# Kernel optimization log

Hardware: AMD Instinct MI355X
Metric: run time of the kernel (lower is better)

The kernel has to match this reference:

```python
import jax, jax.numpy as jnp
import numpy as np

IMAGE_SIZE = 512
STRIDES = (8, 16, 32)
W_SEG, W_DET, W_CLS = 1.0, 1.0, 0.5


def _bce_logits(x, y):
    # numerically stable binary cross entropy with logits (broadcasts y)
    return jnp.maximum(x, 0.0) - x * y + jnp.log1p(jnp.exp(-jnp.abs(x)))


def _focal_loss_mean(logits, targets, num_classes, alpha=0.25, gamma=2.0):
    # sigmoid focal loss; targets are class indices, -1 (or any negative) => all-background row
    t = jax.nn.one_hot(targets, num_classes, dtype=logits.dtype)
    p = jax.nn.sigmoid(logits)
    ce = _bce_logits(logits, t)
    p_t = p * t + (1.0 - p) * (1.0 - t)
    a_t = alpha * t + (1.0 - alpha) * (1.0 - t)
    return jnp.mean(a_t * (1.0 - p_t) ** gamma * ce)


def _det_scale_loss(cls_logits, reg_preds, cent_preds, boxes, labels, stride):
    B, Cp1, H, W = cls_logits.shape
    C = Cp1 - 1
    L = H * W
    cls = jnp.transpose(cls_logits, (0, 2, 3, 1))[..., 1:].reshape(B, L, C)
    reg = jnp.transpose(reg_preds, (0, 2, 3, 1)).reshape(B, L, 4)
    cent = cent_preds.reshape(B, L)
    xs = (jnp.arange(W, dtype=jnp.float32) + 0.5) * stride
    ys = (jnp.arange(H, dtype=jnp.float32) + 0.5) * stride
    gy, gx = jnp.meshgrid(ys, xs, indexing='ij')
    loc_x = gx.reshape(-1)
    loc_y = gy.reshape(-1)

    def per_image(cls_i, reg_i, cent_i, gb, gl):
        b = gb * IMAGE_SIZE  # [cx,cy,w,h] in pixels
        x0 = b[:, 0] - b[:, 2] * 0.5
        y0 = b[:, 1] - b[:, 3] * 0.5
        x1 = b[:, 0] + b[:, 2] * 0.5
        y1 = b[:, 1] + b[:, 3] * 0.5
        l = loc_x[:, None] - x0[None, :]
        t = loc_y[:, None] - y0[None, :]
        r = x1[None, :] - loc_x[:, None]
        btm = y1[None, :] - loc_y[:, None]
        ltrb = jnp.stack([l, t, r, btm], axis=-1)  # (L, N, 4)
        inside = jnp.min(ltrb, axis=-1) > 0
        area = (x1 - x0) * (y1 - y0)
        masked_area = jnp.where(inside, area[None, :], jnp.inf)
        idx = jnp.argmin(masked_area, axis=-1)  # min-area matched box per location
        pos = jnp.any(inside, axis=-1)
        cls_t = jnp.where(pos, gl[idx], -1)
        reg_t = jnp.take_along_axis(ltrb, idx[:, None, None], axis=1)[:, 0, :] / stride
        lr = reg_t[:, jnp.array([0, 2])]
        tb = reg_t[:, jnp.array([1, 3])]
        eps = 1e-6
        cen_t = jnp.sqrt(jnp.clip((jnp.min(lr, -1) / (jnp.max(lr, -1) + eps)) * (jnp.min(tb, -1) / (jnp.max(tb, -1) + eps)), 0.0, 1.0))
        cls_l = _focal_loss_mean(cls_i, cls_t, C)
        npos = jnp.sum(pos)
        d = reg_i - reg_t
        sl1 = jnp.mean(jnp.where(jnp.abs(d) < 1.0, 0.5 * d * d, jnp.abs(d) - 0.5), axis=-1)
        posf = pos.astype(jnp.float32)
        denom = jnp.maximum(npos, 1).astype(jnp.float32)
        reg_l = jnp.where(npos > 0, jnp.sum(sl1 * posf) / denom, 0.0)
        bce = _bce_logits(cent_i, cen_t)
        cen_l = jnp.where(npos > 0, jnp.sum(bce * posf) / denom, 0.0)
        return cls_l, reg_l, cen_l

    cl, rl, cel = jax.vmap(per_image)(cls, reg, cent, boxes, labels)
    return jnp.mean(cl), jnp.mean(rl), jnp.mean(cel)


def _total_loss(seg_logits, seg_mask, cls_list, reg_list, cen_list, boxes, labels, cls_pred, cls_target):
    # segmentation: BCE-with-logits, integer mask broadcast as float target over channels
    seg_t = seg_mask.astype(jnp.float32)[:, None, :, :]  # (B,1,H,W) broadcasts vs (B,C,H,W)
    seg_loss = jnp.mean(_bce_logits(seg_logits, seg_t))
    tot_cls = 0.0
    tot_reg = 0.0
    tot_cen = 0.0
    for s in range(3):
        cl, rl, cel = _det_scale_loss(cls_list[s], reg_list[s], cen_list[s], boxes, labels, STRIDES[s])
        tot_cls = tot_cls + cl
        tot_reg = tot_reg + rl
        tot_cen = tot_cen + cel
    n = 3.0
    det_loss = tot_cls / n + tot_reg / n + tot_cen / n
    cls_loss = _focal_loss_mean(cls_pred, cls_target, cls_pred.shape[-1])
    return W_SEG * seg_loss + W_DET * det_loss + W_CLS * cls_loss


def setup_inputs() -> dict:
    key = jax.random.key(0)
    ks = jax.random.split(key, 16)
    B = 32
    inp = {
        'seg_logits': jax.random.normal(ks[0], (B, 4, 512, 512), jnp.float32),
        'seg_mask': jax.random.randint(ks[1], (B, 512, 512), 0, 4, jnp.int32),
        'cls_logits_s0': jax.random.normal(ks[2], (B, 5, 64, 64), jnp.float32),
        'cls_logits_s1': jax.random.normal(ks[3], (B, 5, 32, 32), jnp.float32),
        'cls_logits_s2': jax.random.normal(ks[4], (B, 5, 16, 16), jnp.float32),
        'reg_preds_s0': jax.random.normal(ks[5], (B, 4, 64, 64), jnp.float32),
        'reg_preds_s1': jax.random.normal(ks[6], (B, 4, 32, 32), jnp.float32),
        'reg_preds_s2': jax.random.normal(ks[7], (B, 4, 16, 16), jnp.float32),
        'centerness_s0': jax.random.normal(ks[8], (B, 1, 64, 64), jnp.float32),
        'centerness_s1': jax.random.normal(ks[9], (B, 1, 32, 32), jnp.float32),
        'centerness_s2': jax.random.normal(ks[10], (B, 1, 16, 16), jnp.float32),
        'boxes': jax.random.uniform(ks[11], (B, 20, 4), jnp.float32),
        'labels': jax.random.randint(ks[12], (B, 20), 0, 4, jnp.int32),
        'cls_pred': jax.random.normal(ks[13], (B, 10), jnp.float32),
        'cls_target': jax.random.randint(ks[14], (B,), 0, 10, jnp.int32),
    }
    return inp


def reference(seg_logits, seg_mask, cls_logits_s0, cls_logits_s1, cls_logits_s2, reg_preds_s0, reg_preds_s1, reg_preds_s2, centerness_s0, centerness_s1, centerness_s2, boxes, labels, cls_pred, cls_target):
    return _total_loss(seg_logits, seg_mask,
                       (cls_logits_s0, cls_logits_s1, cls_logits_s2),
                       (reg_preds_s0, reg_preds_s1, reg_preds_s2),
                       (centerness_s0, centerness_s1, centerness_s2),
                       boxes, labels, cls_pred, cls_target)
```

## Files before the change

### kernel.cpp

```cpp
#include <hip/hip_runtime.h>
#include <math.h>

#define NB 32
#define SEG_BLOCKS 2048
#define DET_BLOCKS 96


__device__ __forceinline__ float bce_logits(float x, float y) {
    float a = fabsf(x);
    return fmaxf(x, 0.f) - x * y + __logf(1.f + __expf(-a));
}

__device__ __forceinline__ float focal_elt(float x, float t) {
    float p = 1.f / (1.f + __expf(-x));
    float ce = bce_logits(x, t);
    float p_t = (t > 0.5f) ? p : (1.f - p);
    float a_t = (t > 0.5f) ? 0.25f : 0.75f;
    float om = 1.f - p_t;
    return a_t * om * om * ce;
}

template <int N>
__device__ void blk_reduce_arr(float* v) {
    __shared__ float sm[N][4];
    int lane = threadIdx.x & 63;
    int wid  = threadIdx.x >> 6;
#pragma unroll
    for (int j = 0; j < N; j++) {
        float x = v[j];
#pragma unroll
        for (int off = 32; off > 0; off >>= 1) x += __shfl_down(x, off, 64);
        if (lane == 0) sm[j][wid] = x;
    }
    __syncthreads();
    if (threadIdx.x == 0) {
#pragma unroll
        for (int j = 0; j < N; j++) {
            float s = 0.f;
#pragma unroll
            for (int w = 0; w < 4; w++) s += sm[j][w];
            v[j] = s;
        }
    }
}


__global__ __launch_bounds__(256) void fused_kernel(
        const float* __restrict__ seg_logits, const int* __restrict__ mask,
        const float* __restrict__ cls0, const float* __restrict__ cls1, const float* __restrict__ cls2,
        const float* __restrict__ reg0, const float* __restrict__ reg1, const float* __restrict__ reg2,
        const float* __restrict__ cen0, const float* __restrict__ cen1, const float* __restrict__ cen2,
        const float* __restrict__ boxes, const int* __restrict__ labels,
        float* __restrict__ segpart, float* __restrict__ detc) {

    if (blockIdx.x < DET_BLOCKS) {
        const int s = blockIdx.x >> 5;
        const int b = blockIdx.x & 31;
        int Wd, shift, L; float stride;
        const float *cls, *reg, *cen;
        if (s == 0)      { Wd = 64; shift = 6; L = 4096; stride = 8.f;  cls = cls0; reg = reg0; cen = cen0; }
        else if (s == 1) { Wd = 32; shift = 5; L = 1024; stride = 16.f; cls = cls1; reg = reg1; cen = cen1; }
        else             { Wd = 16; shift = 4; L = 256;  stride = 32.f; cls = cls2; reg = reg2; cen = cen2; }

        __shared__ float sx0[20], sy0[20], sx1[20], sy1[20], sar[20];
        __shared__ int   slb[20];
        if (threadIdx.x < 20) {
            int k = threadIdx.x;
            const float* bb = boxes + (b * 20 + k) * 4;
            float cx = bb[0] * 512.f, cy = bb[1] * 512.f;
            float w  = bb[2] * 512.f, h  = bb[3] * 512.f;
            float x0 = cx - 0.5f * w, y0 = cy - 0.5f * h;
            float x1 = cx + 0.5f * w, y1 = cy + 0.5f * h;
            sx0[k] = x0; sy0[k] = y0; sx1[k] = x1; sy1[k] = y1;
            sar[k] = (x1 - x0) * (y1 - y0);
            slb[k] = labels[b * 20 + k];
        }
        __syncthreads();

        const float* clsb = cls + (size_t)b * 5 * L;
        const float* regb = reg + (size_t)b * 4 * L;
        const float* cenb = cen + (size_t)b * L;
        const float inv = 1.f / stride;

        float cls_s = 0.f, reg_s = 0.f, cen_s = 0.f, np = 0.f;
        for (int l = threadIdx.x; l < L; l += 256) {
            float lx = ((l & (Wd - 1)) + 0.5f) * stride;
            float ly = ((l >> shift)   + 0.5f) * stride;
            int bk = -1; float ba = INFINITY;
            float bl = 0.f, btp = 0.f, brr = 0.f, bbt = 0.f;
#pragma unroll
            for (int k = 0; k < 20; k++) {
                float li = lx - sx0[k], ti = ly - sy0[k];
                float ri = sx1[k] - lx, bi = sy1[k] - ly;
                float mn = fminf(fminf(li, ti), fminf(ri, bi));
                if (mn > 0.f && sar[k] < ba) {
                    ba = sar[k]; bk = k;
                    bl = li; btp = ti; brr = ri; bbt = bi;
                }
            }
            int tl = (bk >= 0) ? slb[bk] : -1;
#pragma unroll
            for (int c = 0; c < 4; c++) {
                float x = clsb[(c + 1) * L + l];
                cls_s += focal_elt(x, (c == tl) ? 1.f : 0.f);
            }
            if (bk >= 0) {
                float r0 = bl * inv, r1 = btp * inv, r2 = brr * inv, r3 = bbt * inv;
                float d0 = regb[0 * L + l] - r0;
                float d1 = regb[1 * L + l] - r1;
                float d2 = regb[2 * L + l] - r2;
                float d3 = regb[3 * L + l] - r3;
                float a0 = fabsf(d0), a1 = fabsf(d1), a2 = fabsf(d2), a3 = fabsf(d3);
                float sl = (a0 < 1.f ? 0.5f * d0 * d0 : a0 - 0.5f)
                         + (a1 < 1.f ? 0.5f * d1 * d1 : a1 - 0.5f)
                         + (a2 < 1.f ? 0.5f * d2 * d2 : a2 - 0.5f)
                         + (a3 < 1.f ? 0.5f * d3 * d3 : a3 - 0.5f);
                reg_s += 0.25f * sl;
                float mnlr = fminf(r0, r2), mxlr = fmaxf(r0, r2);
                float mntb = fminf(r1, r3), mxtb = fmaxf(r1, r3);
                float v = (mnlr / (mxlr + 1e-6f)) * (mntb / (mxtb + 1e-6f));
                v = fminf(fmaxf(v, 0.f), 1.f);
                float ct = sqrtf(v);
                cen_s += bce_logits(cenb[l], ct);
                np += 1.f;
            }
        }

        float v4[4] = {cls_s, reg_s, cen_s, np};
        blk_reduce_arr<4>(v4);
        if (threadIdx.x == 0) {
            float cls_l = v4[0] / (L * 4.f);
            float npos  = v4[3];
            float denom = fmaxf(npos, 1.f);
            float reg_l = (npos > 0.f) ? v4[1] / denom : 0.f;
            float cen_l = (npos > 0.f) ? v4[2] / denom : 0.f;
            detc[blockIdx.x] = (cls_l + reg_l + cen_l) * (1.f / (float)DET_BLOCKS);
        }
        __syncthreads();
    }

    const int HW  = 512 * 512;
    const int QPI = HW / 4;
    const int TOTQ = NB * QPI;
    int tid = blockIdx.x * 256 + threadIdx.x;
    float acc = 0.f;
    for (int q = tid; q < TOTQ; q += SEG_BLOCKS * 256) {
        int b   = q >> 16;
        int hwq = q & 65535;
        const int4 m4 = ((const int4*)(mask + (size_t)b * HW))[hwq];
        float ty0 = (float)m4.x, ty1 = (float)m4.y, ty2 = (float)m4.z, ty3 = (float)m4.w;
        const float4* base = (const float4*)(seg_logits + (size_t)b * 4 * HW);
#pragma unroll
        for (int c = 0; c < 4; c++) {
            float4 x4 = base[c * QPI + hwq];
            acc += bce_logits(x4.x, ty0) + bce_logits(x4.y, ty1)
                 + bce_logits(x4.z, ty2) + bce_logits(x4.w, ty3);
        }
    }
    float v[1] = {acc};
    blk_reduce_arr<1>(v);
    if (threadIdx.x == 0) segpart[blockIdx.x] = v[0];
}


__global__ __launch_bounds__(256) void final_kernel(
        const float* __restrict__ segpart, const float* __restrict__ detc,
        const float* __restrict__ cls_pred, const int* __restrict__ cls_target,
        float* __restrict__ out) {
    const float seg_scale = 1.f / 33554432.f;
    const float cls_scale = 0.5f / 320.f;
    float acc = 0.f;
    for (int i = threadIdx.x; i < SEG_BLOCKS; i += 256) acc += segpart[i] * seg_scale;
    if (threadIdx.x < DET_BLOCKS) acc += detc[threadIdx.x];
    for (int e = threadIdx.x; e < NB * 10; e += 256) {
        int i = e / 10, c = e - i * 10;
        acc += cls_scale * focal_elt(cls_pred[e], (cls_target[i] == c) ? 1.f : 0.f);
    }
    float v[1] = {acc};
    blk_reduce_arr<1>(v);
    if (threadIdx.x == 0) out[0] = v[0];
}


extern "C" void kernel_launch(void* const* d_in, const int* in_sizes, int n_in,
                              void* d_out, int out_size, void* d_ws, size_t ws_size,
                              hipStream_t stream) {
    const float* seg_logits = (const float*)d_in[0];
    const int*   seg_mask   = (const int*)d_in[1];
    const float* cls0 = (const float*)d_in[2];
    const float* cls1 = (const float*)d_in[3];
    const float* cls2 = (const float*)d_in[4];
    const float* reg0 = (const float*)d_in[5];
    const float* reg1 = (const float*)d_in[6];
    const float* reg2 = (const float*)d_in[7];
    const float* cen0 = (const float*)d_in[8];
    const float* cen1 = (const float*)d_in[9];
    const float* cen2 = (const float*)d_in[10];
    const float* boxes  = (const float*)d_in[11];
    const int*   labels = (const int*)d_in[12];
    const float* cls_pred   = (const float*)d_in[13];
    const int*   cls_target = (const int*)d_in[14];

    float* ws      = (float*)d_ws;
    float* segpart = ws;
    float* detc    = ws + SEG_BLOCKS;

    fused_kernel<<<SEG_BLOCKS, 256, 0, stream>>>(seg_logits, seg_mask,
                                                 cls0, cls1, cls2,
                                                 reg0, reg1, reg2,
                                                 cen0, cen1, cen2,
                                                 boxes, labels, segpart, detc);
    final_kernel<<<1, 256, 0, stream>>>(segpart, detc, cls_pred, cls_target,
                                        (float*)d_out);
}
```

Before: 248.0 us.

## Split detection and segmentation into dedicated blocks and batch segmentation loads

Detection blocks now return after their reduction instead of also doing a share of the segmentation work. The grid grows by the detection block count, and each segmentation block handles one contiguous 1024-quad chunk. Each thread issues all 4 mask loads and 16 logit loads up front before computing, replacing a grid-stride loop, to raise memory-level parallelism. This uses more registers per thread and relies on the total quad count exactly equalling SEG_BLOCKS*1024.

After: 256.7 us. +3.5%, slower.

```diff
diff --git a/kernel.cpp b/kernel.cpp
--- a/kernel.cpp
+++ b/kernel.cpp
@@ -2,8 +2,9 @@
 #include <math.h>
 
 #define NB 32
+#define DET_BLOCKS 96
 #define SEG_BLOCKS 2048
-#define DET_BLOCKS 96
+#define TOTAL_BLOCKS (DET_BLOCKS + SEG_BLOCKS)
 
 
 __device__ __forceinline__ float bce_logits(float x, float y) {
@@ -136,30 +137,44 @@
             float cen_l = (npos > 0.f) ? v4[2] / denom : 0.f;
             detc[blockIdx.x] = (cls_l + reg_l + cen_l) * (1.f / (float)DET_BLOCKS);
         }
-        __syncthreads();
+        return;
     }
 
     const int HW  = 512 * 512;
     const int QPI = HW / 4;
-    const int TOTQ = NB * QPI;
-    int tid = blockIdx.x * 256 + threadIdx.x;
+    const int sblk = blockIdx.x - DET_BLOCKS;
+    const size_t qbase = (size_t)sblk * 1024;
+    const int b   = (int)(qbase >> 16);
+    const int hw0 = (int)(qbase & 65535) + threadIdx.x;
+
+    const int4*   mb = (const int4*)(mask + (size_t)b * HW) + hw0;
+    const float4* xb = (const float4*)(seg_logits + (size_t)b * 4 * HW) + hw0;
+
+    int4   m[4];
+    float4 x[16];
+#pragma unroll
+    for (int u = 0; u < 4; u++) m[u] = mb[u * 256];
+#pragma unroll
+    for (int u = 0; u < 4; u++)
+#pragma unroll
+        for (int c = 0; c < 4; c++) x[u * 4 + c] = xb[c * QPI + u * 256];
+
     float acc = 0.f;
-    for (int q = tid; q < TOTQ; q += SEG_BLOCKS * 256) {
-        int b   = q >> 16;
-        int hwq = q & 65535;
-        const int4 m4 = ((const int4*)(mask + (size_t)b * HW))[hwq];
-        float ty0 = (float)m4.x, ty1 = (float)m4.y, ty2 = (float)m4.z, ty3 = (float)m4.w;
-        const float4* base = (const float4*)(seg_logits + (size_t)b * 4 * HW);
+#pragma unroll
+    for (int u = 0; u < 4; u++) {
+        float ty0 = (float)m[u].x, ty1 = (float)m[u].y;
+        float ty2 = (float)m[u].z, ty3 = (float)m[u].w;
 #pragma unroll
         for (int c = 0; c < 4; c++) {
-            float4 x4 = base[c * QPI + hwq];
-            acc += bce_logits(x4.x, ty0) + bce_logits(x4.y, ty1)
-                 + bce_logits(x4.z, ty2) + bce_logits(x4.w, ty3);
-        }
-    }
+            float4 v = x[u * 4 + c];
+            acc += bce_logits(v.x, ty0) + bce_logits(v.y, ty1)
+                 + bce_logits(v.z, ty2) + bce_logits(v.w, ty3);
+        }
+    }
+
     float v[1] = {acc};
     blk_reduce_arr<1>(v);
-    if (threadIdx.x == 0) segpart[blockIdx.x] = v[0];
+    if (threadIdx.x == 0) segpart[sblk] = v[0];
 }
 
 
@@ -205,11 +220,11 @@
     float* segpart = ws;
     float* detc    = ws + SEG_BLOCKS;
 
-    fused_kernel<<<SEG_BLOCKS, 256, 0, stream>>>(seg_logits, seg_mask,
-                                                 cls0, cls1, cls2,
-                                                 reg0, reg1, reg2,
-                                                 cen0, cen1, cen2,
-                                                 boxes, labels, segpart, detc);
+    fused_kernel<<<TOTAL_BLOCKS, 256, 0, stream>>>(seg_logits, seg_mask,
+                                                   cls0, cls1, cls2,
+                                                   reg0, reg1, reg2,
+                                                   cen0, cen1, cen2,
+                                                   boxes, labels, segpart, detc);
     final_kernel<<<1, 256, 0, stream>>>(segpart, detc, cls_pred, cls_target,
                                         (float*)d_out);
 }
```

## Double-buffer segmentation loads through LDS with async global_load_lds

Applied to the files above, without the earlier changes.

Each segmentation block now owns a contiguous range of 2048 quads. It streams the mask and four logit channels into a double-buffered LDS tile using 16-byte global_load_lds, waiting with explicit vmcnt so the next chunk's loads overlap the current chunk's BCE math. Detection blocks become separate blocks that return early instead of also doing segmentation work, and the grid grows to cover both. The 40KB of shared memory per block limits occupancy, and the hand-written waitcnt and M0 offsets depend on how the compiler orders the loads.

Measured after the change: 247.4 us. No clear change (-0.2%).

```diff
diff --git a/kernel.cpp b/kernel.cpp
--- a/kernel.cpp
+++ b/kernel.cpp
@@ -2,8 +2,10 @@
 #include <math.h>
 
 #define NB 32
-#define SEG_BLOCKS 2048
 #define DET_BLOCKS 96
+#define SEG_BLOCKS 1024
+#define CHUNKS 8
+#define TOTAL_BLOCKS (DET_BLOCKS + SEG_BLOCKS)
 
 
 __device__ __forceinline__ float bce_logits(float x, float y) {
@@ -44,6 +46,11 @@
     }
 }
 
+__device__ __forceinline__ void stage16(const void* g, void* l) {
+    __builtin_amdgcn_global_load_lds((const unsigned int*)g, (unsigned int*)l,
+                                     16, 0, 0);
+}
+
 
 __global__ __launch_bounds__(256) void fused_kernel(
         const float* __restrict__ seg_logits, const int* __restrict__ mask,
@@ -52,6 +59,8 @@
         const float* __restrict__ cen0, const float* __restrict__ cen1, const float* __restrict__ cen2,
         const float* __restrict__ boxes, const int* __restrict__ labels,
         float* __restrict__ segpart, float* __restrict__ detc) {
+
+    __shared__ float4 sbuf[2][5 * 256];
 
     if (blockIdx.x < DET_BLOCKS) {
         const int s = blockIdx.x >> 5;
@@ -136,30 +145,66 @@
             float cen_l = (npos > 0.f) ? v4[2] / denom : 0.f;
             detc[blockIdx.x] = (cls_l + reg_l + cen_l) * (1.f / (float)DET_BLOCKS);
         }
-        __syncthreads();
+        return;
     }
 
     const int HW  = 512 * 512;
     const int QPI = HW / 4;
-    const int TOTQ = NB * QPI;
-    int tid = blockIdx.x * 256 + threadIdx.x;
+    const int sblk = blockIdx.x - DET_BLOCKS;
+    const size_t qbase = (size_t)sblk * 2048;
+    const int b  = (int)(qbase >> 16);
+    const int qs = (int)(qbase & 65535);
+    const int t  = threadIdx.x;
+
+    const int4*   mq = (const int4*)(mask + (size_t)b * HW) + qs;
+    const float4* xq = (const float4*)(seg_logits + (size_t)b * 4 * HW) + qs;
+
+    const int wbyte = __builtin_amdgcn_readfirstlane((t >> 6) << 10);
+
+    #define STAGE(p, j) do {                                                         \
+        char* base = (char*)&sbuf[p][0];                                             \
+        stage16(mq + (j) * 256 + t,           base + 0 * 4096 + wbyte);              \
+        stage16(xq + 0 * QPI + (j) * 256 + t, base + 1 * 4096 + wbyte);              \
+        stage16(xq + 1 * QPI + (j) * 256 + t, base + 2 * 4096 + wbyte);              \
+        stage16(xq + 2 * QPI + (j) * 256 + t, base + 3 * 4096 + wbyte);              \
+        stage16(xq + 3 * QPI + (j) * 256 + t, base + 4 * 4096 + wbyte);              \
+    } while (0)
+
+    STAGE(0, 0);
+
     float acc = 0.f;
-    for (int q = tid; q < TOTQ; q += SEG_BLOCKS * 256) {
-        int b   = q >> 16;
-        int hwq = q & 65535;
-        const int4 m4 = ((const int4*)(mask + (size_t)b * HW))[hwq];
-        float ty0 = (float)m4.x, ty1 = (float)m4.y, ty2 = (float)m4.z, ty3 = (float)m4.w;
-        const float4* base = (const float4*)(seg_logits + (size_t)b * 4 * HW);
-#pragma unroll
-        for (int c = 0; c < 4; c++) {
-            float4 x4 = base[c * QPI + hwq];
-            acc += bce_logits(x4.x, ty0) + bce_logits(x4.y, ty1)
-                 + bce_logits(x4.z, ty2) + bce_logits(x4.w, ty3);
-        }
-    }
+    for (int j = 0; j < CHUNKS; j++) {
+        const int p = j & 1;
+        if (j + 1 < CHUNKS) {
+            STAGE(p ^ 1, j + 1);
+            asm volatile("s_waitcnt vmcnt(5)" ::: "memory");
+        } else {
+            asm volatile("s_waitcnt vmcnt(0)" ::: "memory");
+        }
+        __syncthreads();
+
+        const int4   m  = ((const int4*)&sbuf[p][0])[t];
+        const float4 x0 = sbuf[p][1 * 256 + t];
+        const float4 x1 = sbuf[p][2 * 256 + t];
+        const float4 x2 = sbuf[p][3 * 256 + t];
+        const float4 x3 = sbuf[p][4 * 256 + t];
+        const float t0 = (float)m.x, t1 = (float)m.y, t2 = (float)m.z, t3 = (float)m.w;
+        acc += bce_logits(x0.x, t0) + bce_logits(x0.y, t1)
+             + bce_logits(x0.z, t2) + bce_logits(x0.w, t3);
+        acc += bce_logits(x1.x, t0) + bce_logits(x1.y, t1)
+             + bce_logits(x1.z, t2) + bce_logits(x1.w, t3);
+        acc += bce_logits(x2.x, t0) + bce_logits(x2.y, t1)
+             + bce_logits(x2.z, t2) + bce_logits(x2.w, t3);
+        acc += bce_logits(x3.x, t0) + bce_logits(x3.y, t1)
+             + bce_logits(x3.z, t2) + bce_logits(x3.w, t3);
+
+        __syncthreads();
+    }
+    #undef STAGE
+
     float v[1] = {acc};
     blk_reduce_arr<1>(v);
-    if (threadIdx.x == 0) segpart[blockIdx.x] = v[0];
+    if (threadIdx.x == 0) segpart[sblk] = v[0];
 }
 
 
@@ -205,11 +250,11 @@
     float* segpart = ws;
     float* detc    = ws + SEG_BLOCKS;
 
-    fused_kernel<<<SEG_BLOCKS, 256, 0, stream>>>(seg_logits, seg_mask,
-                                                 cls0, cls1, cls2,
-                                                 reg0, reg1, reg2,
-                                                 cen0, cen1, cen2,
-                                                 boxes, labels, segpart, detc);
+    fused_kernel<<<TOTAL_BLOCKS, 256, 0, stream>>>(seg_logits, seg_mask,
+                                                   cls0, cls1, cls2,
+                                                   reg0, reg1, reg2,
+                                                   cen0, cen1, cen2,
+                                                   boxes, labels, segpart, detc);
     final_kernel<<<1, 256, 0, stream>>>(segpart, detc, cls_pred, cls_target,
                                         (float*)d_out);
 }
```

## Split fused kernel into separate seg and det kernels with one-shot seg blocks

Applied to the files above, without the earlier changes.

The fused kernel, in which the first 96 blocks also handled detection, is split into a dedicated segmentation kernel and a detection kernel launched back-to-back. The segmentation kernel now uses 8192 blocks where each thread handles exactly one float4 group with no grid-stride loop, and it carries occupancy launch bounds. The goal is to stop detection blocks from delaying the segmentation stream and to expose more memory-level parallelism. In exchange there is an extra kernel launch, the detection work is serialized after the seg kernel instead of overlapping with it, and the final reduction has four times as many partial sums to add.

After: 271.3 us. +9.4%, slower.

```diff
diff --git a/kernel.cpp b/kernel.cpp
--- a/kernel.cpp
+++ b/kernel.cpp
@@ -2,8 +2,8 @@
 #include <math.h>
 
 #define NB 32
-#define SEG_BLOCKS 2048
 #define DET_BLOCKS 96
+#define SEG_BLOCKS 8192
 
 
 __device__ __forceinline__ float bce_logits(float x, float y) {
@@ -45,121 +45,127 @@
 }
 
 
-__global__ __launch_bounds__(256) void fused_kernel(
-        const float* __restrict__ seg_logits, const int* __restrict__ mask,
+__global__ __launch_bounds__(256, 8) void seg_kernel(
+        const float* __restrict__ logits, const int* __restrict__ mask,
+        float* __restrict__ partial) {
+    const int HW  = 512 * 512;
+    const int QPI = HW / 4;
+    const int b  = blockIdx.x >> 8;
+    const int hw = ((blockIdx.x & 255) << 8) + threadIdx.x;
+
+    const int4 m4 = ((const int4*)(mask + (size_t)b * HW))[hw];
+    const float4* xb = (const float4*)(logits + (size_t)b * 4 * HW) + hw;
+    const float4 x0 = xb[0];
+    const float4 x1 = xb[QPI];
+    const float4 x2 = xb[2 * QPI];
+    const float4 x3 = xb[3 * QPI];
+
+    const float t0 = (float)m4.x, t1 = (float)m4.y;
+    const float t2 = (float)m4.z, t3 = (float)m4.w;
+    float acc;
+    acc  = bce_logits(x0.x, t0) + bce_logits(x0.y, t1)
+         + bce_logits(x0.z, t2) + bce_logits(x0.w, t3);
+    acc += bce_logits(x1.x, t0) + bce_logits(x1.y, t1)
+         + bce_logits(x1.z, t2) + bce_logits(x1.w, t3);
+    acc += bce_logits(x2.x, t0) + bce_logits(x2.y, t1)
+         + bce_logits(x2.z, t2) + bce_logits(x2.w, t3);
+    acc += bce_logits(x3.x, t0) + bce_logits(x3.y, t1)
+         + bce_logits(x3.z, t2) + bce_logits(x3.w, t3);
+
+    float v[1] = {acc};
+    blk_reduce_arr<1>(v);
+    if (threadIdx.x == 0) partial[blockIdx.x] = v[0];
+}
+
+
+__global__ __launch_bounds__(256) void det_kernel(
         const float* __restrict__ cls0, const float* __restrict__ cls1, const float* __restrict__ cls2,
         const float* __restrict__ reg0, const float* __restrict__ reg1, const float* __restrict__ reg2,
         const float* __restrict__ cen0, const float* __restrict__ cen1, const float* __restrict__ cen2,
         const float* __restrict__ boxes, const int* __restrict__ labels,
-        float* __restrict__ segpart, float* __restrict__ detc) {
-
-    if (blockIdx.x < DET_BLOCKS) {
-        const int s = blockIdx.x >> 5;
-        const int b = blockIdx.x & 31;
-        int Wd, shift, L; float stride;
-        const float *cls, *reg, *cen;
-        if (s == 0)      { Wd = 64; shift = 6; L = 4096; stride = 8.f;  cls = cls0; reg = reg0; cen = cen0; }
-        else if (s == 1) { Wd = 32; shift = 5; L = 1024; stride = 16.f; cls = cls1; reg = reg1; cen = cen1; }
-        else             { Wd = 16; shift = 4; L = 256;  stride = 32.f; cls = cls2; reg = reg2; cen = cen2; }
-
-        __shared__ float sx0[20], sy0[20], sx1[20], sy1[20], sar[20];
-        __shared__ int   slb[20];
-        if (threadIdx.x < 20) {
-            int k = threadIdx.x;
-            const float* bb = boxes + (b * 20 + k) * 4;
-            float cx = bb[0] * 512.f, cy = bb[1] * 512.f;
-            float w  = bb[2] * 512.f, h  = bb[3] * 512.f;
-            float x0 = cx - 0.5f * w, y0 = cy - 0.5f * h;
-            float x1 = cx + 0.5f * w, y1 = cy + 0.5f * h;
-            sx0[k] = x0; sy0[k] = y0; sx1[k] = x1; sy1[k] = y1;
-            sar[k] = (x1 - x0) * (y1 - y0);
-            slb[k] = labels[b * 20 + k];
-        }
-        __syncthreads();
-
-        const float* clsb = cls + (size_t)b * 5 * L;
-        const float* regb = reg + (size_t)b * 4 * L;
-        const float* cenb = cen + (size_t)b * L;
-        const float inv = 1.f / stride;
-
-        float cls_s = 0.f, reg_s = 0.f, cen_s = 0.f, np = 0.f;
-        for (int l = threadIdx.x; l < L; l += 256) {
-            float lx = ((l & (Wd - 1)) + 0.5f) * stride;
-            float ly = ((l >> shift)   + 0.5f) * stride;
-            int bk = -1; float ba = INFINITY;
-            float bl = 0.f, btp = 0.f, brr = 0.f, bbt = 0.f;
-#pragma unroll
-            for (int k = 0; k < 20; k++) {
-                float li = lx - sx0[k], ti = ly - sy0[k];
-                float ri = sx1[k] - lx, bi = sy1[k] - ly;
-                float mn = fminf(fminf(li, ti), fminf(ri, bi));
-                if (mn > 0.f && sar[k] < ba) {
-                    ba = sar[k]; bk = k;
-                    bl = li; btp = ti; brr = ri; bbt = bi;
-                }
+        float* __restrict__ detc) {
+    const int s = blockIdx.x >> 5;
+    const int b = blockIdx.x & 31;
+    int Wd, shift, L; float stride;
+    const float *cls, *reg, *cen;
+    if (s == 0)      { Wd = 64; shift = 6; L = 4096; stride = 8.f;  cls = cls0; reg = reg0; cen = cen0; }
+    else if (s == 1) { Wd = 32; shift = 5; L = 1024; stride = 16.f; cls = cls1; reg = reg1; cen = cen1; }
+    else             { Wd = 16; shift = 4; L = 256;  stride = 32.f; cls = cls2; reg = reg2; cen = cen2; }
+
+    __shared__ float sx0[20], sy0[20], sx1[20], sy1[20], sar[20];
+    __shared__ int   slb[20];
+    if (threadIdx.x < 20) {
+        int k = threadIdx.x;
+        const float* bb = boxes + (b * 20 + k) * 4;
+        float cx = bb[0] * 512.f, cy = bb[1] * 512.f;
+        float w  = bb[2] * 512.f, h  = bb[3] * 512.f;
+        float x0 = cx - 0.5f * w, y0 = cy - 0.5f * h;
+        float x1 = cx + 0.5f * w, y1 = cy + 0.5f * h;
+        sx0[k] = x0; sy0[k] = y0; sx1[k] = x1; sy1[k] = y1;
+        sar[k] = (x1 - x0) * (y1 - y0);
+        slb[k] = labels[b * 20 + k];
+    }
+    __syncthreads();
+
+    const float* clsb = cls + (size_t)b * 5 * L;
+    const float* regb = reg + (size_t)b * 4 * L;
+    const float* cenb = cen + (size_t)b * L;
+    const float inv = 1.f / stride;
+
+    float cls_s = 0.f, reg_s = 0.f, cen_s = 0.f, np = 0.f;
+    for (int l = threadIdx.x; l < L; l += 256) {
+        float lx = ((l & (Wd - 1)) + 0.5f) * stride;
+        float ly = ((l >> shift)   + 0.5f) * stride;
+        int bk = -1; float ba = INFINITY;
+        float bl = 0.f, btp = 0.f, brr = 0.f, bbt = 0.f;
+#pragma unroll
+        for (int k = 0; k < 20; k++) {
+            float li = lx - sx0[k], ti = ly - sy0[k];
+            float ri = sx1[k] - lx, bi = sy1[k] - ly;
+            float mn = fminf(fminf(li, ti), fminf(ri, bi));
+            if (mn > 0.f && sar[k] < ba) {
+                ba = sar[k]; bk = k;
+                bl = li; btp = ti; brr = ri; bbt = bi;
             }
-            int tl = (bk >= 0) ? slb[bk] : -1;
-#pragma unroll
-            for (int c = 0; c < 4; c++) {
-                float x = clsb[(c + 1) * L + l];
-                cls_s += focal_elt(x, (c == tl) ? 1.f : 0.f);
-            }
-            if (bk >= 0) {
-                float r0 = bl * inv, r1 = btp * inv, r2 = brr * inv, r3 = bbt * inv;
-                float d0 = regb[0 * L + l] - r0;
-                float d1 = regb[1 * L + l] - r1;
-                float d2 = regb[2 * L + l] - r2;
-                float d3 = regb[3 * L + l] - r3;
-                float a0 = fabsf(d0), a1 = fabsf(d1), a2 = fabsf(d2), a3 = fabsf(d3);
-                float sl = (a0 < 1.f ? 0.5f * d0 * d0 : a0 - 0.5f)
-                         + (a1 < 1.f ? 0.5f * d1 * d1 : a1 - 0.5f)
-                         + (a2 < 1.f ? 0.5f * d2 * d2 : a2 - 0.5f)
-                         + (a3 < 1.f ? 0.5f * d3 * d3 : a3 - 0.5f);
-                reg_s += 0.25f * sl;
-                float mnlr = fminf(r0, r2), mxlr = fmaxf(r0, r2);
-                float mntb = fminf(r1, r3), mxtb = fmaxf(r1, r3);
-                float v = (mnlr / (mxlr + 1e-6f)) * (mntb / (mxtb + 1e-6f));
-                v = fminf(fmaxf(v, 0.f), 1.f);
-                float ct = sqrtf(v);
-                cen_s += bce_logits(cenb[l], ct);
-                np += 1.f;
-            }
-        }
-
-        float v4[4] = {cls_s, reg_s, cen_s, np};
-        blk_reduce_arr<4>(v4);
-        if (threadIdx.x == 0) {
-            float cls_l = v4[0] / (L * 4.f);
-            float npos  = v4[3];
-            float denom = fmaxf(npos, 1.f);
-            float reg_l = (npos > 0.f) ? v4[1] / denom : 0.f;
-            float cen_l = (npos > 0.f) ? v4[2] / denom : 0.f;
-            detc[blockIdx.x] = (cls_l + reg_l + cen_l) * (1.f / (float)DET_BLOCKS);
-        }
-        __syncthreads();
-    }
-
-    const int HW  = 512 * 512;
-    const int QPI = HW / 4;
-    const int TOTQ = NB * QPI;
-    int tid = blockIdx.x * 256 + threadIdx.x;
-    float acc = 0.f;
-    for (int q = tid; q < TOTQ; q += SEG_BLOCKS * 256) {
-        int b   = q >> 16;
-        int hwq = q & 65535;
-        const int4 m4 = ((const int4*)(mask + (size_t)b * HW))[hwq];
-        float ty0 = (float)m4.x, ty1 = (float)m4.y, ty2 = (float)m4.z, ty3 = (float)m4.w;
-        const float4* base = (const float4*)(seg_logits + (size_t)b * 4 * HW);
+        }
+        int tl = (bk >= 0) ? slb[bk] : -1;
 #pragma unroll
         for (int c = 0; c < 4; c++) {
-            float4 x4 = base[c * QPI + hwq];
-            acc += bce_logits(x4.x, ty0) + bce_logits(x4.y, ty1)
-                 + bce_logits(x4.z, ty2) + bce_logits(x4.w, ty3);
-        }
-    }
-    float v[1] = {acc};
-    blk_reduce_arr<1>(v);
-    if (threadIdx.x == 0) segpart[blockIdx.x] = v[0];
+            float x = clsb[(c + 1) * L + l];
+            cls_s += focal_elt(x, (c == tl) ? 1.f : 0.f);
+        }
+        if (bk >= 0) {
+            float r0 = bl * inv, r1 = btp * inv, r2 = brr * inv, r3 = bbt * inv;
+            float d0 = regb[0 * L + l] - r0;
+            float d1 = regb[1 * L + l] - r1;
+            float d2 = regb[2 * L + l] - r2;
+            float d3 = regb[3 * L + l] - r3;
+            float a0 = fabsf(d0), a1 = fabsf(d1), a2 = fabsf(d2), a3 = fabsf(d3);
+            float sl = (a0 < 1.f ? 0.5f * d0 * d0 : a0 - 0.5f)
+                     + (a1 < 1.f ? 0.5f * d1 * d1 : a1 - 0.5f)
+                     + (a2 < 1.f ? 0.5f * d2 * d2 : a2 - 0.5f)
+                     + (a3 < 1.f ? 0.5f * d3 * d3 : a3 - 0.5f);
+            reg_s += 0.25f * sl;
+            float mnlr = fminf(r0, r2), mxlr = fmaxf(r0, r2);
+            float mntb = fminf(r1, r3), mxtb = fmaxf(r1, r3);
+            float v = (mnlr / (mxlr + 1e-6f)) * (mntb / (mxtb + 1e-6f));
+            v = fminf(fmaxf(v, 0.f), 1.f);
+            float ct = sqrtf(v);
+            cen_s += bce_logits(cenb[l], ct);
+            np += 1.f;
+        }
+    }
+
+    float v4[4] = {cls_s, reg_s, cen_s, np};
+    blk_reduce_arr<4>(v4);
+    if (threadIdx.x == 0) {
+        float cls_l = v4[0] / (L * 4.f);
+        float npos  = v4[3];
+        float denom = fmaxf(npos, 1.f);
+        float reg_l = (npos > 0.f) ? v4[1] / denom : 0.f;
+        float cen_l = (npos > 0.f) ? v4[2] / denom : 0.f;
+        detc[blockIdx.x] = (cls_l + reg_l + cen_l) * (1.f / (float)DET_BLOCKS);
+    }
 }
 
 
@@ -205,11 +211,11 @@
     float* segpart = ws;
     float* detc    = ws + SEG_BLOCKS;
 
-    fused_kernel<<<SEG_BLOCKS, 256, 0, stream>>>(seg_logits, seg_mask,
-                                                 cls0, cls1, cls2,
-                                                 reg0, reg1, reg2,
-                                                 cen0, cen1, cen2,
-                                                 boxes, labels, segpart, detc);
+    seg_kernel<<<SEG_BLOCKS, 256, 0, stream>>>(seg_logits, seg_mask, segpart);
+    det_kernel<<<DET_BLOCKS, 256, 0, stream>>>(cls0, cls1, cls2,
+                                               reg0, reg1, reg2,
+                                               cen0, cen1, cen2,
+                                               boxes, labels, detc);
     final_kernel<<<1, 256, 0, stream>>>(segpart, detc, cls_pred, cls_target,
                                         (float*)d_out);
 }
```
